# Kernel tuning notes

Measured on AMD Instinct MI355X. Metric: run time of the kernel, lower is better.

The kernel has to match this reference:

```python
import jax, jax.numpy as jnp
import numpy as np


def setup_inputs() -> dict:
    key = jax.random.key(0)
    N0, N1, N2, E0, E1 = 40000, 8000, 2000, 128000, 32000
    IN, HID = 512, 256
    ks = iter(jax.random.split(key, 40))
    def nk():
        return next(ks)
    def lin_w(shape):
        fan_in = shape[1]
        return jax.random.uniform(nk(), shape, jnp.float32, -1.0, 1.0) / np.sqrt(fan_in)
    inp = {}
    inp["x"] = jax.random.normal(nk(), (N0, IN), jnp.float32)
    inp["ppr"] = jax.random.uniform(nk(), (N1, N1), jnp.float32) / N1  # ~row-stochastic PPR
    inp["src0"] = jax.random.randint(nk(), (E0,), 0, N0)
    inp["dst0"] = jax.random.randint(nk(), (E0,), 0, N1)
    inp["src1"] = jax.random.randint(nk(), (E1,), 0, N1)
    inp["dst1"] = jax.random.randint(nk(), (E1,), 0, N2)
    inp["n1"] = N1
    inp["n2"] = N2
    # SAGEConv layer 0 (in->hid) and layer 1 (hid->hid); lin_l has bias, lin_r does not (PyG default)
    inp["Wl0"] = lin_w((HID, IN)); inp["bl0"] = jnp.zeros((HID,), jnp.float32); inp["Wr0"] = lin_w((HID, IN))
    inp["Wl1"] = lin_w((HID, HID)); inp["bl1"] = jnp.zeros((HID,), jnp.float32); inp["Wr1"] = lin_w((HID, HID))
    # self.linear = [Linear(IN,IN)+ReLU, Linear(IN,HID)]
    inp["Wa"] = lin_w((IN, IN)); inp["ba"] = jnp.zeros((IN,), jnp.float32)
    inp["Wb"] = lin_w((HID, IN)); inp["bb"] = jnp.zeros((HID,), jnp.float32)
    # lin1 / lin2 (no bias)
    inp["W1"] = lin_w((HID, HID)); inp["W2"] = lin_w((HID, HID))
    # proj = MLP(HID, HID, HID)
    inp["Wp1"] = lin_w((HID, HID)); inp["bp1"] = jnp.zeros((HID,), jnp.float32)
    inp["Wp2"] = lin_w((HID, HID)); inp["bp2"] = jnp.zeros((HID,), jnp.float32)
    # clf = MLP(HID, 32, 1)
    inp["Wc1"] = lin_w((32, HID)); inp["bc1"] = jnp.zeros((32,), jnp.float32)
    inp["Wc2"] = lin_w((1, 32)); inp["bc2"] = jnp.zeros((1,), jnp.float32)
    return inp


def reference(x, ppr, Wl0, bl0, Wr0, Wl1, bl1, Wr1, Wa, ba, Wb, bb,
              W1, W2, Wp1, bp1, Wp2, bp2, Wc1, bc1, Wc2, bc2,
              src0, dst0, src1, dst1, n1, n2):
    EPS = 1e-12
    def l2n(v):
        return v / jnp.maximum(jnp.linalg.norm(v, axis=-1, keepdims=True), EPS)
    def sage(h_src, h_tgt, src, dst, Wl, bl, Wr, n_tgt):
        msg = h_src[src]  # [E, d] gather
        s = jax.ops.segment_sum(msg, dst, num_segments=n_tgt)
        cnt = jax.ops.segment_sum(jnp.ones((dst.shape[0],), h_src.dtype), dst, num_segments=n_tgt)
        agg = s / jnp.maximum(cnt, 1.0)[:, None]  # scatter-mean
        return agg @ Wl.T + bl + h_tgt @ Wr.T
    # --- GraphSAGE encoder (eval mode: dropout no-op) ---
    h = x
    h = sage(h, h[:n1], src0, dst0, Wl0, bl0, Wr0, n1)
    h = jax.nn.relu(h)
    h = sage(h, h[:n2], src1, dst1, Wl1, bl1, Wr1, n2)
    ebds = jax.nn.log_softmax(h, axis=-1)  # output_type 'ebds' != 'ebd' -> log_softmax path
    # --- divergence loss ---
    o1 = l2n(ebds @ W1.T)
    o2 = l2n(ebds @ W2.T)
    div_loss = jnp.mean(jnp.sum((o1 - o2) ** 2, axis=-1))
    # --- PPR branch ---
    xp = ppr[:n1, :n1] @ x[:n1]              # [n1, IN]
    xp = jax.nn.relu(xp @ Wa.T + ba)         # linear[0]
    xp = ppr[:n2, :n2] @ xp[:n2]             # [n2, IN]
    xp = xp @ Wb.T + bb                      # linear[1] -> [n2, HID]
    g1 = l2n(ebds)
    g2 = l2n(xp)
    def proj(v):
        return jax.nn.relu(v @ Wp1.T + bp1) @ Wp2.T + bp2
    def clf(v):
        return jax.nn.relu(v @ Wc1.T + bc1) @ Wc2.T + bc2
    l1 = clf(proj(g1))  # [n2, 1]
    l2_ = clf(proj(g2))  # [n2, 1]
    logits_pair = jnp.concatenate([l1, l2_], axis=-1)  # [n2, 2]
    return logits_pair, div_loss
```

## Files before the change

### kernel.cpp

```cpp
#include <hip/hip_runtime.h>


typedef unsigned short ushort;
typedef __attribute__((ext_vector_type(8))) short short8;
typedef __attribute__((ext_vector_type(4))) float float4v;
typedef __attribute__((ext_vector_type(4))) float f32x4;
typedef __attribute__((ext_vector_type(2))) float f32x2;
typedef __attribute__((ext_vector_type(8))) unsigned short us8;
typedef __attribute__((ext_vector_type(4))) unsigned short us4;
typedef __attribute__((ext_vector_type(2))) unsigned short us2;

__device__ __forceinline__ ushort bf16_rne(float v) {
    unsigned u = __float_as_uint(v);
    u += 0x7fffu + ((u >> 16) & 1u);
    return (ushort)(u >> 16);
}
__device__ __forceinline__ float bf16_f32(ushort h) {
    return __uint_as_float((unsigned)h << 16);
}

constexpr long ZCNT0 = 0;
constexpr long ZCNT1 = 8000;
constexpr long ELL0  = 10240;
constexpr long ELL1  = 522240;
constexpr long H1F   = 650240;
constexpr long H2F   = 2714624;
constexpr long DIVCF = 3238912;
constexpr long PB2   = 4811776;
constexpr long PART  = 5860352;
constexpr long FEND  = 10054656;
constexpr long U_PPRB  = 0;
constexpr long U_PPR2B = 16777216;
constexpr long U_XTB   = 20971520;
constexpr long U_XPATB = 25165824;
constexpr long U_A0    = 26214400;
constexpr long U_A1    = 38600704;
constexpr long U_ESPL  = 40697856;
constexpr long U_XPS   = 41746432;
constexpr long U_SPLT  = 43843584;
constexpr long U_TSPL  = 45940736;
constexpr long U_WC0   = 48037888;
constexpr long U_WC1   = 48431104;
constexpr long U_BD    = 48693248;
constexpr long U_WAD   = 48955392;
constexpr long U_WBD   = 49479680;
constexpr long U_WP1D  = 49741824;
constexpr long U_WP2D  = 49872896;
constexpr long U_XB    = 50003968;

struct GemmDesc {
    const ushort* A; const ushort* B;
    float* Cf; ushort* Cs; ushort* Ct;
    const float* bias;
    int K, lda, ldb, ldc;
    int ldso, nsplit, msplit, ldt;
    int gx, gy, kchunk;
    long slabsize;
    int flags;
};

__device__ __forceinline__ void run_gemm(const GemmDesc& d, int f,
                                         ushort* As, ushort* Bs)
{
    const int tid = threadIdx.x;
    const int lane = tid & 63, wave = tid >> 6;
    const int wm = (wave >> 1) * 64, wn = (wave & 1) * 64;
    const int lr = lane & 15, quad = lane >> 4;

    int per = d.gx * d.gy;
    int z = f / per;
    int rem = f - z * per;
    if (d.flags & 8) {
        int c = rem & 7, j = rem >> 3;
        rem = c * (per >> 3) + j;
    }
    int by = rem / d.gx, bx = rem - by * d.gx;
    const int bm = by * 128, bn = bx * 128;
    const int kbeg = z * d.kchunk;
    int kend = kbeg + d.kchunk; if (kend > d.K) kend = d.K;

    float4v acc[4][4] = {{{0.f, 0.f, 0.f, 0.f}}};

    for (int k0 = kbeg; k0 < kend; k0 += 128) {
#pragma unroll
        for (int issue = 0; issue < 8; ++issue) {
            int c = issue * 256 + tid;
            int r = c >> 4, p = c & 15;
            int kk = (p ^ (r & 15)) * 8;
            const ushort* ga = d.A + (long)(bm + r) * d.lda + k0 + kk;
            const ushort* gb = d.B + (long)(bn + r) * d.ldb + k0 + kk;
            __builtin_amdgcn_global_load_lds(
                (const __attribute__((address_space(1))) unsigned int*)ga,
                (__attribute__((address_space(3))) unsigned int*)&As[c * 8], 16, 0, 0);
            __builtin_amdgcn_global_load_lds(
                (const __attribute__((address_space(1))) unsigned int*)gb,
                (__attribute__((address_space(3))) unsigned int*)&Bs[c * 8], 16, 0, 0);
        }
        __syncthreads();

#pragma unroll
        for (int s = 0; s < 4; ++s) {
            short8 af[4], bf[4];
#pragma unroll
            for (int i = 0; i < 4; ++i) {
                int ra = wm + i * 16 + lr;
                af[i] = *(const short8*)&As[ra * 128 + (((s * 4 + quad) ^ (ra & 15)) * 8)];
                int rb = wn + i * 16 + lr;
                bf[i] = *(const short8*)&Bs[rb * 128 + (((s * 4 + quad) ^ (rb & 15)) * 8)];
            }
#pragma unroll
            for (int i = 0; i < 4; ++i)
#pragma unroll
                for (int j = 0; j < 4; ++j)
                    acc[i][j] = __builtin_amdgcn_mfma_f32_16x16x32_bf16(
                        af[i], bf[j], acc[i][j], 0, 0, 0);
        }
        __syncthreads();
    }

    if (d.flags & 16) {
        float* Cz = d.Cf + (long)z * d.slabsize;
#pragma unroll
        for (int i = 0; i < 4; ++i) {
            int row0 = bm + wm + i * 16 + quad * 4;
#pragma unroll
            for (int j = 0; j < 4; ++j) {
                int col = bn + wn + j * 16 + lr;
#pragma unroll
                for (int r = 0; r < 4; ++r)
                    Cz[(long)(row0 + r) * d.ldc + col] = acc[i][j][r];
            }
        }
        return;
    }

#pragma unroll
    for (int i = 0; i < 4; ++i) {
        int row0 = bm + wm + i * 16 + quad * 4;
#pragma unroll
        for (int j = 0; j < 4; ++j) {
            int col = bn + wn + j * 16 + lr;
            float bv = d.bias ? d.bias[col] : 0.f;
            us4 tp;
#pragma unroll
            for (int r = 0; r < 4; ++r) {
                int row = row0 + r;
                float v = acc[i][j][r] + bv;
                if (d.flags & 1) v = fmaxf(v, 0.f);
                if (d.Cf) d.Cf[(long)row * d.ldc + col] = v;
                if (d.Cs && row < d.msplit) {
                    if (d.flags & 2) {
                        ushort h = bf16_rne(v);
                        d.Cs[(long)row * d.ldso + col] = h;
                        d.Cs[(long)row * d.ldso + d.nsplit + col] = bf16_rne(v - bf16_f32(h));
                    } else {
                        d.Cs[(long)row * d.ldso + col] = bf16_rne(v);
                    }
                }
                if (d.flags & 4) tp[r] = bf16_rne(v);
            }
            if (d.flags & 4)
                *(us4*)&d.Ct[(long)col * d.ldt + row0] = tp;
        }
    }
}

__device__ __forceinline__ void run_gemm_norm(const GemmDesc& d, int f,
                                              ushort* As, ushort* Bs)
{
    const int tid = threadIdx.x;
    const int lane = tid & 63, wave = tid >> 6;
    const int wm = (wave >> 1) * 64, wn = (wave & 1) * 64;
    const int lr = lane & 15, quad = lane >> 4;
    const int bm = f * 128;

    float4v acc[2][4][4] = {{{{0.f, 0.f, 0.f, 0.f}}}};

#pragma unroll 2
    for (int tile = 0; tile < 2; ++tile) {
        for (int k0 = 0; k0 < d.K; k0 += 128) {
#pragma unroll
            for (int issue = 0; issue < 8; ++issue) {
                int c = issue * 256 + tid;
                int r = c >> 4, p = c & 15;
                int kk = (p ^ (r & 15)) * 8;
                const ushort* ga = d.A + (long)(bm + r) * d.lda + k0 + kk;
                const ushort* gb = d.B + (long)(tile * 128 + r) * d.ldb + k0 + kk;
                __builtin_amdgcn_global_load_lds(
                    (const __attribute__((address_space(1))) unsigned int*)ga,
                    (__attribute__((address_space(3))) unsigned int*)&As[c * 8], 16, 0, 0);
                __builtin_amdgcn_global_load_lds(
                    (const __attribute__((address_space(1))) unsigned int*)gb,
                    (__attribute__((address_space(3))) unsigned int*)&Bs[c * 8], 16, 0, 0);
            }
            __syncthreads();
#pragma unroll
            for (int s = 0; s < 4; ++s) {
                short8 af[4], bf[4];
#pragma unroll
                for (int i = 0; i < 4; ++i) {
                    int ra = wm + i * 16 + lr;
                    af[i] = *(const short8*)&As[ra * 128 + (((s * 4 + quad) ^ (ra & 15)) * 8)];
                    int rb = wn + i * 16 + lr;
                    bf[i] = *(const short8*)&Bs[rb * 128 + (((s * 4 + quad) ^ (rb & 15)) * 8)];
                }
#pragma unroll
                for (int i = 0; i < 4; ++i)
#pragma unroll
                    for (int j = 0; j < 4; ++j)
                        acc[tile][i][j] = __builtin_amdgcn_mfma_f32_16x16x32_bf16(
                            af[i], bf[j], acc[tile][i][j], 0, 0, 0);
            }
            __syncthreads();
        }
    }

    float* rs = (float*)As;
    if (tid < 128) rs[tid] = 0.f;
    __syncthreads();
#pragma unroll
    for (int i = 0; i < 4; ++i) {
#pragma unroll
        for (int r = 0; r < 4; ++r) {
            int rl = wm + i * 16 + quad * 4 + r;
            float p = 0.f;
#pragma unroll
            for (int j = 0; j < 4; ++j) {
                int c0 = wn + j * 16 + lr;
                float v0 = acc[0][i][j][r] + d.bias[c0];
                float v1 = acc[1][i][j][r] + d.bias[128 + c0];
                acc[0][i][j][r] = v0;
                acc[1][i][j][r] = v1;
                p += v0 * v0 + v1 * v1;
            }
            atomicAdd(&rs[rl], p);
        }
    }
    __syncthreads();
#pragma unroll
    for (int i = 0; i < 4; ++i) {
#pragma unroll
        for (int r = 0; r < 4; ++r) {
            int rl = wm + i * 16 + quad * 4 + r;
            float inv = 1.f / fmaxf(sqrtf(rs[rl]), 1e-12f);
            long ro = (long)(bm + rl) * 512;
#pragma unroll
            for (int j = 0; j < 4; ++j) {
                int c0 = wn + j * 16 + lr;
                float g0 = acc[0][i][j][r] * inv;
                float g1 = acc[1][i][j][r] * inv;
                ushort h0 = bf16_rne(g0), h1 = bf16_rne(g1);
                d.Cs[ro + c0] = h0;
                d.Cs[ro + 256 + c0] = bf16_rne(g0 - bf16_f32(h0));
                d.Cs[ro + 128 + c0] = h1;
                d.Cs[ro + 256 + 128 + c0] = bf16_rne(g1 - bf16_f32(h1));
            }
        }
    }
}

__device__ __forceinline__ void reduce4_body(
    const float* __restrict__ part, ushort* __restrict__ outs, long j, int S)
{
    if (j >= 262144) return;
    long i4 = j * 4;
    f32x4 s = {0.f, 0.f, 0.f, 0.f};
    for (int k = 0; k < S; ++k)
        s += *(const f32x4*)&part[(long)k * 1048576 + i4];
    int r = (int)(i4 >> 9), c = (int)(i4 & 511);
    us4 hi, lo;
#pragma unroll
    for (int q = 0; q < 4; ++q) {
        ushort h = bf16_rne(s[q]);
        hi[q] = h;
        lo[q] = bf16_rne(s[q] - bf16_f32(h));
    }
    *(us4*)&outs[(long)r * 1024 + c] = hi;
    *(us4*)&outs[(long)r * 1024 + 512 + c] = lo;
}

__global__ __launch_bounds__(256) void gemm_one(GemmDesc d)
{
    __shared__ ushort As[16384];
    __shared__ ushort Bs[16384];
    run_gemm(d, blockIdx.x, As, Bs);
}

__global__ __launch_bounds__(256) void gemm_dual(GemmDesc d0, int n0, GemmDesc d1)
{
    __shared__ ushort As[16384];
    __shared__ ushort Bs[16384];
    int f = blockIdx.x;
    if (f < n0) run_gemm(d0, f, As, Bs);
    else if (d1.flags & 32) run_gemm_norm(d1, f - n0, As, Bs);
    else run_gemm(d1, f - n0, As, Bs);
}

__global__ __launch_bounds__(256) void aggred(
    const float* __restrict__ h, const int* __restrict__ ell,
    const int* __restrict__ cnt, ushort* __restrict__ a1,
    const float* __restrict__ part, ushort* __restrict__ outs)
{
    __shared__ float pl[4][256];
    int b = blockIdx.x, t = threadIdx.x;
    if (b >= 2048) {
        reduce4_body(part, outs, (long)(b - 2048) * 256 + t, 4);
        return;
    }
    int d = b;
    int w = t >> 6, lane = t & 63;
    int k = (d < 2000) ? min(cnt[d], 64) : 0;
    f32x4 s = {0.f, 0.f, 0.f, 0.f};
    int co = lane * 4;
    int j = w;
    for (; j + 12 < k; j += 16) {
        int e0 = ell[d + 2000 * j],        e1 = ell[d + 2000 * (j + 4)];
        int e2 = ell[d + 2000 * (j + 8)],  e3 = ell[d + 2000 * (j + 12)];
        f32x4 v0 = *(const f32x4*)&h[(long)e0 * 256 + co];
        f32x4 v1 = *(const f32x4*)&h[(long)e1 * 256 + co];
        f32x4 v2 = *(const f32x4*)&h[(long)e2 * 256 + co];
        f32x4 v3 = *(const f32x4*)&h[(long)e3 * 256 + co];
        s += v0; s += v1; s += v2; s += v3;
    }
    for (; j < k; j += 4)
        s += *(const f32x4*)&h[(long)ell[d + 2000 * j] * 256 + co];
#pragma unroll
    for (int q = 0; q < 4; ++q) pl[w][co + q] = s[q];
    __syncthreads();
    float inv = 1.f / fmaxf((float)k, 1.f);
    float a = (pl[0][t] + pl[1][t] + pl[2][t] + pl[3][t]) * inv;
    ushort hi = bf16_rne(a);
    long ro = (long)d * 1024;
    a1[ro + 512 + t] = hi;
    a1[ro + 768 + t] = bf16_rne(a - bf16_f32(hi));
}

__global__ __launch_bounds__(256) void auxdual2(
    const float* __restrict__ h2, ushort* __restrict__ espl,
    ushort* __restrict__ splt,
    const float* __restrict__ part, ushort* __restrict__ outs)
{
    __shared__ float red[256];
    int b = blockIdx.x, t = threadIdx.x;
    if (b >= 2000) {
        reduce4_body(part, outs, (long)(b - 2000) * 256 + t, 2);
        return;
    }
    int i = b;
    float v = h2[(long)i * 256 + t];
    red[t] = v;
    __syncthreads();
    for (int s = 128; s > 0; s >>= 1) {
        if (t < s) red[t] = fmaxf(red[t], red[t + s]);
        __syncthreads();
    }
    float m = red[0];
    __syncthreads();
    float e = expf(v - m);
    red[t] = e;
    __syncthreads();
    for (int s = 128; s > 0; s >>= 1) {
        if (t < s) red[t] += red[t + s];
        __syncthreads();
    }
    float eb = v - (m + logf(red[0]));
    ushort hh = bf16_rne(eb);
    espl[(long)i * 512 + t] = hh;
    espl[(long)i * 512 + 256 + t] = bf16_rne(eb - bf16_f32(hh));
    __syncthreads();
    red[t] = eb * eb;
    __syncthreads();
    for (int s = 128; s > 0; s >>= 1) {
        if (t < s) red[t] += red[t + s];
        __syncthreads();
    }
    float g = eb / fmaxf(sqrtf(red[0]), 1e-12f);
    ushort gh = bf16_rne(g);
    splt[(long)i * 512 + t] = gh;
    splt[(long)i * 512 + 256 + t] = bf16_rne(g - bf16_f32(gh));
}

__global__ __launch_bounds__(256) void prep(
    const float* __restrict__ ppr, const float* __restrict__ x,
    const float* __restrict__ Wr0, const float* __restrict__ Wl0,
    const float* __restrict__ Wr1, const float* __restrict__ Wl1,
    const float* __restrict__ W1,  const float* __restrict__ W2,
    const float* __restrict__ Wa,  const float* __restrict__ Wb,
    const float* __restrict__ Wp1, const float* __restrict__ Wp2,
    const int* __restrict__ src0, const int* __restrict__ dst0,
    const int* __restrict__ src1, const int* __restrict__ dst1,
    int E0, int E1,
    ushort* __restrict__ uws, int* __restrict__ iws, float* __restrict__ outloss)
{
    __shared__ float tsm[32][33];
    int b = blockIdx.x, t = threadIdx.x;
    int nEll = (E0 + E1 + 255) >> 8;

    if (b < nEll) {
        int e = b * 256 + t;
        if (e < E0) {
            int d = dst0[e];
            int r = atomicAdd(&iws[ZCNT0 + d], 1);
            if (r < 64) iws[ELL0 + d + 8000 * r] = src0[e];
        } else if (e < E0 + E1) {
            int e1 = e - E0;
            int d = dst1[e1];
            int r = atomicAdd(&iws[ZCNT1 + d], 1);
            if (r < 64) iws[ELL1 + d + 2000 * r] = src1[e1];
        }
        return;
    }
    int b1 = b - nEll;
    if (b1 == 0) {
        if (t == 0) outloss[0] = 0.f;
        return;
    }
    b1 -= 1;
    if (b1 < 256) {
        int b2 = b1;
        int sec = b2 >> 5;
        const float *sa, *sb = nullptr; long dstoff; int N, KA, dA, KB = 0, dB = 0;
        switch (sec) {
            case 0: sa = Wr0; KA = 512; dA = 1; sb = Wl0; KB = 512; dB = 2;
                    dstoff = U_WC0; N = 256; break;
            case 1: sa = Wr1; KA = 256; dA = 2; sb = Wl1; KB = 256; dB = 2;
                    dstoff = U_WC1; N = 256; break;
            case 2: sa = W1;  KA = 256; dA = 2; dstoff = U_BD;          N = 256; break;
            case 3: sa = W2;  KA = 256; dA = 2; dstoff = U_BD + 131072; N = 256; break;
            case 4: sa = Wa;  KA = 512; dA = 2; dstoff = U_WAD;  N = 512; break;
            case 5: sa = Wb;  KA = 512; dA = 2; dstoff = U_WBD;  N = 256; break;
            case 6: sa = Wp1; KA = 256; dA = 2; dstoff = U_WP1D; N = 256; break;
            default: sa = Wp2; KA = 256; dA = 2; dstoff = U_WP2D; N = 256; break;
        }
        int kd = KA * dA + KB * dB;
        long totv = (long)N * kd / 2;
        for (long v = (long)(b2 & 31) * 256 + t; v < totv; v += 8192) {
            long idx = v * 2;
            int n = (int)(idx / kd), rem = (int)(idx % kd);
            f32x2 val;
            if (rem < KA * dA) {
                int sc = rem % KA;
                val = *(const f32x2*)&sa[(long)n * KA + sc];
            } else {
                int sc = (rem - KA * dA) % KB;
                val = *(const f32x2*)&sb[(long)n * KB + sc];
            }
            us2 o; o[0] = bf16_rne(val[0]); o[1] = bf16_rne(val[1]);
            *(us2*)&uws[dstoff + idx] = o;
        }
        return;
    }
    b1 -= 256;
    if (b1 < 8192) {
        int r = b1 >> 2, q = b1 & 3;
        bool live = r < 2000;
        const float* row = ppr + (long)r * 8000;
        int cbeg = q * 2048;
#pragma unroll
        for (int pass = 0; pass < 2; ++pass) {
            int c = cbeg + pass * 1024 + t * 4;
            f32x4 v = {0.f, 0.f, 0.f, 0.f};
            if (live && c < 8000) v = *(const f32x4*)(row + c);
            us4 u;
            u[0] = bf16_rne(v[0]); u[1] = bf16_rne(v[1]);
            u[2] = bf16_rne(v[2]); u[3] = bf16_rne(v[3]);
            *(us4*)&uws[U_PPRB + (long)r * 8192 + c] = u;
            if (c < 2048) {
                us4 w = u;
                if (c >= 2000) { w[0] = 0; w[1] = 0; w[2] = 0; w[3] = 0; }
                *(us4*)&uws[U_PPR2B + (long)r * 2048 + c] = w;
            }
        }
        return;
    }
    b1 -= 8192;
    if (b1 < 4096) {
        int c0 = (b1 & 15) * 32, r0 = (b1 >> 4) * 32;
        int tx = t & 31, ty = t >> 5;
#pragma unroll
        for (int k = 0; k < 32; k += 8) {
            int r = r0 + ty + k;
            tsm[ty + k][tx] = (r < 8000) ? x[(long)r * 512 + c0 + tx] : 0.f;
        }
        __syncthreads();
#pragma unroll
        for (int k = 0; k < 32; k += 8) {
            int c = c0 + ty + k;
            uws[U_XTB + (long)c * 8192 + r0 + tx] = bf16_rne(tsm[tx][ty + k]);
        }
        return;
    }
    b1 -= 4096;
    {
        long vi = (long)b1 * 256 + t;
        for (; vi < 5120000; vi += 327680) {
            long gidx = vi * 4;
            f32x4 v = *(const f32x4*)&x[gidx];
            us4 u;
            u[0] = bf16_rne(v[0]); u[1] = bf16_rne(v[1]);
            u[2] = bf16_rne(v[2]); u[3] = bf16_rne(v[3]);
            *(us4*)&uws[U_XB + gidx] = u;
            long row = gidx >> 9;
            if (row < 8064) {
                int col = (int)(gidx & 511);
                *(us4*)&uws[U_A0 + row * 1536 + col] = u;
            }
        }
    }
}

__global__ __launch_bounds__(256) void csr_agg0(
    const ushort* __restrict__ xb, const int* __restrict__ ell,
    const int* __restrict__ cnt, ushort* __restrict__ a0)
{
    __shared__ float part[4][512];
    int d = blockIdx.x, t = threadIdx.x;
    int w = t >> 6, lane = t & 63;
    int k = (d < 8000) ? min(cnt[d], 64) : 0;
    float s[8] = {0.f, 0.f, 0.f, 0.f, 0.f, 0.f, 0.f, 0.f};
    int co = lane * 8;
    int j = w;
    for (; j + 12 < k; j += 16) {
        int e0 = ell[d + 8000 * j],        e1 = ell[d + 8000 * (j + 4)];
        int e2 = ell[d + 8000 * (j + 8)],  e3 = ell[d + 8000 * (j + 12)];
        us8 v0 = *(const us8*)&xb[(long)e0 * 512 + co];
        us8 v1 = *(const us8*)&xb[(long)e1 * 512 + co];
        us8 v2 = *(const us8*)&xb[(long)e2 * 512 + co];
        us8 v3 = *(const us8*)&xb[(long)e3 * 512 + co];
#pragma unroll
        for (int q = 0; q < 8; ++q)
            s[q] += bf16_f32(v0[q]) + bf16_f32(v1[q]) +
                    bf16_f32(v2[q]) + bf16_f32(v3[q]);
    }
    for (; j < k; j += 4) {
        us8 v = *(const us8*)&xb[(long)ell[d + 8000 * j] * 512 + co];
#pragma unroll
        for (int q = 0; q < 8; ++q) s[q] += bf16_f32(v[q]);
    }
#pragma unroll
    for (int q = 0; q < 8; ++q) part[w][co + q] = s[q];
    __syncthreads();
    float inv = 1.f / fmaxf((float)k, 1.f);
    long ro = (long)d * 1536;
#pragma unroll
    for (int h = 0; h < 2; ++h) {
        int c = 2 * t + h;
        float a = (part[0][c] + part[1][c] + part[2][c] + part[3][c]) * inv;
        ushort hi = bf16_rne(a);
        a0[ro + 512 + c] = hi;
        a0[ro + 1024 + c] = bf16_rne(a - bf16_f32(hi));
    }
}

__global__ __launch_bounds__(256) void final_combo(
    const float* __restrict__ p, const float* __restrict__ Wc1,
    const float* __restrict__ bc1, const float* __restrict__ Wc2,
    const float* __restrict__ bc2, float* __restrict__ out,
    const float* __restrict__ divc, float scale)
{
    __shared__ float v[256];
    __shared__ float ps[8][33];
    __shared__ float hsum[32];
    __shared__ float r2[256];
    int b = blockIdx.x, t = threadIdx.x;
    if (b >= 4096) {
        int i = b - 4096;
        float a = divc[(long)i * 512 + t], bb = divc[(long)i * 512 + 256 + t];
        v[t] = a * a;
        r2[t] = bb * bb;
        __syncthreads();
        for (int s = 128; s > 0; s >>= 1) {
            if (t < s) { v[t] += v[t + s]; r2[t] += r2[t + s]; }
            __syncthreads();
        }
        float na = fmaxf(sqrtf(v[0]), 1e-12f);
        float nb = fmaxf(sqrtf(r2[0]), 1e-12f);
        __syncthreads();
        float d = a / na - bb / nb;
        v[t] = d * d;
        __syncthreads();
        for (int s = 128; s > 0; s >>= 1) {
            if (t < s) v[t] += v[t + s];
            __syncthreads();
        }
        if (t == 0) atomicAdd(&out[4000], v[0] * scale);
        return;
    }
    int half = b >> 11, i = b & 2047;
    if (i >= 2000) return;
    v[t] = p[(long)b * 256 + t];
    __syncthreads();
    int o = t & 31, ch = t >> 5;
    const float* w = Wc1 + (long)o * 256 + ch * 32;
    const float* vv = v + ch * 32;
    float s = 0.f;
#pragma unroll
    for (int k2 = 0; k2 < 32; ++k2) s += vv[k2] * w[k2];
    ps[ch][o] = s;
    __syncthreads();
    if (t < 32) {
        float a = bc1[t];
#pragma unroll
        for (int c = 0; c < 8; ++c) a += ps[c][t];
        a = fmaxf(a, 0.f);
        hsum[t] = a * Wc2[t];
    }
    __syncthreads();
    if (t == 0) {
        float s2 = bc2[0];
        for (int k2 = 0; k2 < 32; ++k2) s2 += hsum[k2];
        out[(long)i * 2 + half] = s2;
    }
}

extern "C" void kernel_launch(void* const* d_in, const int* in_sizes, int n_in,
                              void* d_out, int out_size, void* d_ws, size_t ws_size,
                              hipStream_t stream)
{
    constexpr int N2 = 2000;

    const float* x   = (const float*)d_in[0];
    const float* ppr = (const float*)d_in[1];
    const int* src0  = (const int*)d_in[2];
    const int* dst0  = (const int*)d_in[3];
    const int* src1  = (const int*)d_in[4];
    const int* dst1  = (const int*)d_in[5];
    const float* Wl0 = (const float*)d_in[8];
    const float* bl0 = (const float*)d_in[9];
    const float* Wr0 = (const float*)d_in[10];
    const float* Wl1 = (const float*)d_in[11];
    const float* bl1 = (const float*)d_in[12];
    const float* Wr1 = (const float*)d_in[13];
    const float* Wa  = (const float*)d_in[14];
    const float* ba  = (const float*)d_in[15];
    const float* Wb  = (const float*)d_in[16];
    const float* bb  = (const float*)d_in[17];
    const float* W1  = (const float*)d_in[18];
    const float* W2  = (const float*)d_in[19];
    const float* Wp1 = (const float*)d_in[20];
    const float* bp1 = (const float*)d_in[21];
    const float* Wp2 = (const float*)d_in[22];
    const float* bp2 = (const float*)d_in[23];
    const float* Wc1 = (const float*)d_in[24];
    const float* bc1 = (const float*)d_in[25];
    const float* Wc2 = (const float*)d_in[26];
    const float* bc2 = (const float*)d_in[27];

    const int E0 = in_sizes[2];
    const int E1 = in_sizes[4];

    float* out = (float*)d_out;
    float* ws  = (float*)d_ws;
    int*   iws = (int*)d_ws;
    ushort* uws = (ushort*)((char*)d_ws + FEND * sizeof(float));

    GemmDesc z{};

    hipMemsetAsync(iws, 0, 10240 * sizeof(int), stream);

    int nEll = (E0 + E1 + 255) / 256;
    int prepGrid = nEll + 1 + 256 + 8192 + 4096 + 1280;
    prep<<<prepGrid, 256, 0, stream>>>(ppr, x, Wr0, Wl0, Wr1, Wl1, W1, W2,
                                       Wa, Wb, Wp1, Wp2,
                                       src0, dst0, src1, dst1, E0, E1,
                                       uws, iws, out + (long)N2 * 2);

    csr_agg0<<<8064, 256, 0, stream>>>(uws + U_XB, iws + ELL0, iws + ZCNT0,
                                       uws + U_A0);

    GemmDesc dxp1 = z;
    dxp1.A = uws + U_PPRB; dxp1.B = uws + U_XTB; dxp1.Cf = ws + PART;
    dxp1.K = 8192; dxp1.lda = 8192; dxp1.ldb = 8192; dxp1.ldc = 512;
    dxp1.gx = 4; dxp1.gy = 16; dxp1.kchunk = 2048; dxp1.slabsize = 1048576;
    dxp1.flags = 16 | 8;
    GemmDesc dh1 = z;
    dh1.A = uws + U_A0; dh1.B = uws + U_WC0; dh1.Cf = ws + H1F;
    dh1.Cs = uws + U_A1; dh1.bias = bl0;
    dh1.K = 1536; dh1.lda = 1536; dh1.ldb = 1536; dh1.ldc = 256;
    dh1.ldso = 1024; dh1.nsplit = 256; dh1.msplit = 2048;
    dh1.gx = 2; dh1.gy = 63; dh1.kchunk = 1536; dh1.flags = 3;
    gemm_dual<<<382, 256, 0, stream>>>(dxp1, 256, dh1);

    aggred<<<3072, 256, 0, stream>>>(ws + H1F, iws + ELL1, iws + ZCNT1,
                                     uws + U_A1, ws + PART, uws + U_XPS);

    GemmDesc dxpa = z;
    dxpa.A = uws + U_XPS; dxpa.B = uws + U_WAD; dxpa.Ct = uws + U_XPATB;
    dxpa.bias = ba;
    dxpa.K = 1024; dxpa.lda = 1024; dxpa.ldb = 1024; dxpa.ldt = 2048;
    dxpa.gx = 4; dxpa.gy = 16; dxpa.kchunk = 1024; dxpa.flags = 1 | 4 | 8;
    GemmDesc dh2 = z;
    dh2.A = uws + U_A1; dh2.B = uws + U_WC1; dh2.Cf = ws + H2F; dh2.bias = bl1;
    dh2.K = 1024; dh2.lda = 1024; dh2.ldb = 1024; dh2.ldc = 256;
    dh2.gx = 2; dh2.gy = 16; dh2.kchunk = 1024; dh2.flags = 8;
    gemm_dual<<<96, 256, 0, stream>>>(dxpa, 64, dh2);

    GemmDesc dxp2 = z;
    dxp2.A = uws + U_PPR2B; dxp2.B = uws + U_XPATB; dxp2.Cf = ws + PART;
    dxp2.K = 2048; dxp2.lda = 2048; dxp2.ldb = 2048; dxp2.ldc = 512;
    dxp2.gx = 4; dxp2.gy = 16; dxp2.kchunk = 1024; dxp2.slabsize = 1048576;
    dxp2.flags = 16 | 8;
    gemm_one<<<128, 256, 0, stream>>>(dxp2);

    auxdual2<<<3024, 256, 0, stream>>>(ws + H2F, uws + U_ESPL, uws + U_SPLT,
                                       ws + PART, uws + U_XPS);

    GemmDesc ddiv = z;
    ddiv.A = uws + U_ESPL; ddiv.B = uws + U_BD; ddiv.Cf = ws + DIVCF;
    ddiv.K = 512; ddiv.lda = 512; ddiv.ldb = 512; ddiv.ldc = 512;
    ddiv.gx = 4; ddiv.gy = 16; ddiv.kchunk = 512; ddiv.flags = 8;
    GemmDesc dnorm = z;
    dnorm.A = uws + U_XPS; dnorm.B = uws + U_WBD;
    dnorm.Cs = uws + U_SPLT + (long)2048 * 512;
    dnorm.bias = bb;
    dnorm.K = 1024; dnorm.lda = 1024; dnorm.ldb = 1024;
    dnorm.flags = 32;
    gemm_dual<<<80, 256, 0, stream>>>(ddiv, 64, dnorm);

    GemmDesc dp1 = z;
    dp1.A = uws + U_SPLT; dp1.B = uws + U_WP1D; dp1.Cs = uws + U_TSPL;
    dp1.bias = bp1;
    dp1.K = 512; dp1.lda = 512; dp1.ldb = 512;
    dp1.ldso = 512; dp1.nsplit = 256; dp1.msplit = 4096;
    dp1.gx = 2; dp1.gy = 32; dp1.kchunk = 512; dp1.flags = 1 | 2 | 8;
    gemm_one<<<64, 256, 0, stream>>>(dp1);

    GemmDesc dp2 = z;
    dp2.A = uws + U_TSPL; dp2.B = uws + U_WP2D; dp2.Cf = ws + PB2;
    dp2.bias = bp2;
    dp2.K = 512; dp2.lda = 512; dp2.ldb = 512; dp2.ldc = 256;
    dp2.gx = 2; dp2.gy = 32; dp2.kchunk = 512; dp2.flags = 8;
    gemm_one<<<64, 256, 0, stream>>>(dp2);

    final_combo<<<6096, 256, 0, stream>>>(ws + PB2, Wc1, bc1, Wc2, bc2, out,
                                          ws + DIVCF, 1.0f / N2);
}
```

Measured before the change: 694.2 us.

## Reschedule tail GEMMs to co-launch independent branch work across kernels

Moves the log-softmax/normalize row kernel ahead of the second PPR GEMM and splits the proj MLP GEMMs into the ebds half and the xp half. The ebds half now runs in the same launch as the PPR GEMM and the divergence GEMM (gemm_tri), and later beside the norm GEMM. This is meant to fill idle CUs in small, under-occupied launches by running independent branches together. In exchange the reduce becomes its own launch and the xp-half proj GEMMs run as two extra small launches, so the launch count and the serial dependencies change.

```diff
diff --git a/kernel.cpp b/kernel.cpp
--- a/kernel.cpp
+++ b/kernel.cpp
@@ -292,8 +292,34 @@
     __shared__ ushort Bs[16384];
     int f = blockIdx.x;
     if (f < n0) run_gemm(d0, f, As, Bs);
-    else if (d1.flags & 32) run_gemm_norm(d1, f - n0, As, Bs);
-    else run_gemm(d1, f - n0, As, Bs);
+    else        run_gemm(d1, f - n0, As, Bs);
+}
+
+__global__ __launch_bounds__(256) void gemm_tri(
+    GemmDesc d0, int n0, GemmDesc d1, int n1, GemmDesc d2)
+{
+    __shared__ ushort As[16384];
+    __shared__ ushort Bs[16384];
+    int f = blockIdx.x;
+    if (f < n0)           run_gemm(d0, f, As, Bs);
+    else if (f < n0 + n1) run_gemm(d1, f - n0, As, Bs);
+    else                  run_gemm(d2, f - n0 - n1, As, Bs);
+}
+
+__global__ __launch_bounds__(256) void gemm_normdual(
+    GemmDesc dn, int n0, GemmDesc d1)
+{
+    __shared__ ushort As[16384];
+    __shared__ ushort Bs[16384];
+    int f = blockIdx.x;
+    if (f < n0) run_gemm_norm(dn, f, As, Bs);
+    else        run_gemm(d1, f - n0, As, Bs);
+}
+
+__global__ __launch_bounds__(256) void reduce_split(
+    const float* __restrict__ part, ushort* __restrict__ outs, int S)
+{
+    reduce4_body(part, outs, (long)blockIdx.x * 256 + threadIdx.x, S);
 }
 
 __global__ __launch_bounds__(256) void aggred(
@@ -333,51 +359,6 @@
     long ro = (long)d * 1024;
     a1[ro + 512 + t] = hi;
     a1[ro + 768 + t] = bf16_rne(a - bf16_f32(hi));
-}
-
-__global__ __launch_bounds__(256) void auxdual2(
-    const float* __restrict__ h2, ushort* __restrict__ espl,
-    ushort* __restrict__ splt,
-    const float* __restrict__ part, ushort* __restrict__ outs)
-{
-    __shared__ float red[256];
-    int b = blockIdx.x, t = threadIdx.x;
-    if (b >= 2000) {
-        reduce4_body(part, outs, (long)(b - 2000) * 256 + t, 2);
-        return;
-    }
-    int i = b;
-    float v = h2[(long)i * 256 + t];
-    red[t] = v;
-    __syncthreads();
-    for (int s = 128; s > 0; s >>= 1) {
-        if (t < s) red[t] = fmaxf(red[t], red[t + s]);
-        __syncthreads();
-    }
-    float m = red[0];
-    __syncthreads();
-    float e = expf(v - m);
-    red[t] = e;
-    __syncthreads();
-    for (int s = 128; s > 0; s >>= 1) {
-        if (t < s) red[t] += red[t + s];
-        __syncthreads();
-    }
-    float eb = v - (m + logf(red[0]));
-    ushort hh = bf16_rne(eb);
-    espl[(long)i * 512 + t] = hh;
-    espl[(long)i * 512 + 256 + t] = bf16_rne(eb - bf16_f32(hh));
-    __syncthreads();
-    red[t] = eb * eb;
-    __syncthreads();
-    for (int s = 128; s > 0; s >>= 1) {
-        if (t < s) red[t] += red[t + s];
-        __syncthreads();
-    }
-    float g = eb / fmaxf(sqrtf(red[0]), 1e-12f);
-    ushort gh = bf16_rne(g);
-    splt[(long)i * 512 + t] = gh;
-    splt[(long)i * 512 + 256 + t] = bf16_rne(g - bf16_f32(gh));
 }
 
 __global__ __launch_bounds__(256) void prep(
@@ -550,6 +531,45 @@
         a0[ro + 512 + c] = hi;
         a0[ro + 1024 + c] = bf16_rne(a - bf16_f32(hi));
     }
+}
+
+__global__ __launch_bounds__(256) void rowcombo1(
+    const float* __restrict__ h2, ushort* __restrict__ espl,
+    ushort* __restrict__ splt)
+{
+    __shared__ float red[256];
+    int i = blockIdx.x, t = threadIdx.x;
+    float v = h2[(long)i * 256 + t];
+    red[t] = v;
+    __syncthreads();
+    for (int s = 128; s > 0; s >>= 1) {
+        if (t < s) red[t] = fmaxf(red[t], red[t + s]);
+        __syncthreads();
+    }
+    float m = red[0];
+    __syncthreads();
+    float e = expf(v - m);
+    red[t] = e;
+    __syncthreads();
+    for (int s = 128; s > 0; s >>= 1) {
+        if (t < s) red[t] += red[t + s];
+        __syncthreads();
+    }
+    float eb = v - (m + logf(red[0]));
+    ushort hh = bf16_rne(eb);
+    espl[(long)i * 512 + t] = hh;
+    espl[(long)i * 512 + 256 + t] = bf16_rne(eb - bf16_f32(hh));
+    __syncthreads();
+    red[t] = eb * eb;
+    __syncthreads();
+    for (int s = 128; s > 0; s >>= 1) {
+        if (t < s) red[t] += red[t + s];
+        __syncthreads();
+    }
+    float g = eb / fmaxf(sqrtf(red[0]), 1e-12f);
+    ushort gh = bf16_rne(g);
+    splt[(long)i * 512 + t] = gh;
+    splt[(long)i * 512 + 256 + t] = bf16_rne(g - bf16_f32(gh));
 }
 
 __global__ __launch_bounds__(256) void final_combo(
@@ -695,42 +715,48 @@
     dh2.gx = 2; dh2.gy = 16; dh2.kchunk = 1024; dh2.flags = 8;
     gemm_dual<<<96, 256, 0, stream>>>(dxpa, 64, dh2);
 
+    rowcombo1<<<N2, 256, 0, stream>>>(ws + H2F, uws + U_ESPL, uws + U_SPLT);
+
     GemmDesc dxp2 = z;
     dxp2.A = uws + U_PPR2B; dxp2.B = uws + U_XPATB; dxp2.Cf = ws + PART;
     dxp2.K = 2048; dxp2.lda = 2048; dxp2.ldb = 2048; dxp2.ldc = 512;
     dxp2.gx = 4; dxp2.gy = 16; dxp2.kchunk = 1024; dxp2.slabsize = 1048576;
     dxp2.flags = 16 | 8;
-    gemm_one<<<128, 256, 0, stream>>>(dxp2);
-
-    auxdual2<<<3024, 256, 0, stream>>>(ws + H2F, uws + U_ESPL, uws + U_SPLT,
-                                       ws + PART, uws + U_XPS);
-
     GemmDesc ddiv = z;
     ddiv.A = uws + U_ESPL; ddiv.B = uws + U_BD; ddiv.Cf = ws + DIVCF;
     ddiv.K = 512; ddiv.lda = 512; ddiv.ldb = 512; ddiv.ldc = 512;
     ddiv.gx = 4; ddiv.gy = 16; ddiv.kchunk = 512; ddiv.flags = 8;
+    GemmDesc dp1a = z;
+    dp1a.A = uws + U_SPLT; dp1a.B = uws + U_WP1D; dp1a.Cs = uws + U_TSPL;
+    dp1a.bias = bp1;
+    dp1a.K = 512; dp1a.lda = 512; dp1a.ldb = 512;
+    dp1a.ldso = 512; dp1a.nsplit = 256; dp1a.msplit = 2048;
+    dp1a.gx = 2; dp1a.gy = 16; dp1a.kchunk = 512; dp1a.flags = 1 | 2 | 8;
+    gemm_tri<<<224, 256, 0, stream>>>(dxp2, 128, ddiv, 64, dp1a);
+
+    reduce_split<<<1024, 256, 0, stream>>>(ws + PART, uws + U_XPS, 2);
+
     GemmDesc dnorm = z;
     dnorm.A = uws + U_XPS; dnorm.B = uws + U_WBD;
     dnorm.Cs = uws + U_SPLT + (long)2048 * 512;
     dnorm.bias = bb;
     dnorm.K = 1024; dnorm.lda = 1024; dnorm.ldb = 1024;
-    dnorm.flags = 32;
-    gemm_dual<<<80, 256, 0, stream>>>(ddiv, 64, dnorm);
-
-    GemmDesc dp1 = z;
-    dp1.A = uws + U_SPLT; dp1.B = uws + U_WP1D; dp1.Cs = uws + U_TSPL;
-    dp1.bias = bp1;
-    dp1.K = 512; dp1.lda = 512; dp1.ldb = 512;
-    dp1.ldso = 512; dp1.nsplit = 256; dp1.msplit = 4096;
-    dp1.gx = 2; dp1.gy = 32; dp1.kchunk = 512; dp1.flags = 1 | 2 | 8;
-    gemm_one<<<64, 256, 0, stream>>>(dp1);
-
-    GemmDesc dp2 = z;
-    dp2.A = uws + U_TSPL; dp2.B = uws + U_WP2D; dp2.Cf = ws + PB2;
-    dp2.bias = bp2;
-    dp2.K = 512; dp2.lda = 512; dp2.ldb = 512; dp2.ldc = 256;
-    dp2.gx = 2; dp2.gy = 32; dp2.kchunk = 512; dp2.flags = 8;
-    gemm_one<<<64, 256, 0, stream>>>(dp2);
+    GemmDesc dp2a = z;
+    dp2a.A = uws + U_TSPL; dp2a.B = uws + U_WP2D; dp2a.Cf = ws + PB2;
+    dp2a.bias = bp2;
+    dp2a.K = 512; dp2a.lda = 512; dp2a.ldb = 512; dp2a.ldc = 256;
+    dp2a.gx = 2; dp2a.gy = 16; dp2a.kchunk = 512; dp2a.flags = 8;
+    gemm_normdual<<<48, 256, 0, stream>>>(dnorm, 16, dp2a);
+
+    GemmDesc dp1b = dp1a;
+    dp1b.A = uws + U_SPLT + (long)2048 * 512;
+    dp1b.Cs = uws + U_TSPL + (long)2048 * 512;
+    gemm_one<<<32, 256, 0, stream>>>(dp1b);
+
+    GemmDesc dp2b = dp2a;
+    dp2b.A = uws + U_TSPL + (long)2048 * 512;
+    dp2b.Cf = ws + PB2 + (long)2048 * 256;
+    gemm_one<<<32, 256, 0, stream>>>(dp2b);
 
     final_combo<<<6096, 256, 0, stream>>>(ws + PB2, Wc1, bc1, Wc2, bc2, out,
                                           ws + DIVCF, 1.0f / N2);
```

Result: no change. 686.6 us (-1.1%).
